# Performance work log

Hardware: AMD Instinct MI355X
Metric: run time of the kernel (lower is better)

## Reference

```python
import jax, jax.numpy as jnp
import numpy as np

E = 1024
H = 16
D = E // H  # head_dim = 64


def setup_inputs() -> dict:
    key = jax.random.key(0)
    ks = jax.random.split(key, 9)
    s = 1.0 / np.sqrt(E)
    inp = {
        "x": jax.random.normal(ks[0], (4, 2048, E), dtype=jnp.float32),
        "Wq": jax.random.uniform(ks[1], (E, E), jnp.float32, -s, s),
        "bq": jax.random.uniform(ks[2], (E,), jnp.float32, -s, s),
        "Wk": jax.random.uniform(ks[3], (E, E), jnp.float32, -s, s),
        "bk": jax.random.uniform(ks[4], (E,), jnp.float32, -s, s),
        "Wv": jax.random.uniform(ks[5], (E, E), jnp.float32, -s, s),
        "bv": jax.random.uniform(ks[6], (E,), jnp.float32, -s, s),
        "Wo": jax.random.uniform(ks[7], (E, E), jnp.float32, -s, s),
        "bo": jax.random.uniform(ks[8], (E,), jnp.float32, -s, s),
    }
    return inp


def reference(x, Wq, bq, Wk, bk, Wv, bv, Wo, bo):
    B, S, _ = x.shape
    scale = D ** -0.5
    # projections (torch Linear: x @ W.T + b), reshape to [B,H,S,D]
    def proj(W, b):
        y = jnp.einsum('bse,fe->bsf', x, W) + b
        return y.reshape(B, S, H, D).transpose(0, 2, 1, 3)
    q = proj(Wq, bq)
    k = proj(Wk, bk)
    v = proj(Wv, bv)
    scores = jnp.einsum('bhsd,bhtd->bhst', q, k) * scale  # [B,H,S,S]
    attn = jax.nn.softmax(scores, axis=-1)
    ctx = jnp.einsum('bhst,bhtd->bhsd', attn, v)  # [B,H,S,D]
    ctx = ctx.transpose(0, 2, 1, 3).reshape(B, S, E)
    out = jnp.einsum('bse,fe->bsf', ctx, Wo) + bo
    attn_avg = attn.mean(axis=1)  # [B,S,S]
    return out, attn_avg
```

## Files before the change

### kernel.cpp

```cpp
#include <hip/hip_runtime.h>
#include <math.h>

#define B_ 4
#define S_ 2048
#define E_ 1024
#define H_ 16
#define D_ 64

typedef __attribute__((ext_vector_type(8))) short bf16x8;
typedef __attribute__((ext_vector_type(4))) short bf16x4;
typedef __attribute__((ext_vector_type(4))) float f32x4;

#define MFMA(a, b, c) __builtin_amdgcn_mfma_f32_16x16x32_bf16((a), (b), (c), 0, 0, 0)

static __device__ __forceinline__ short f2bf(float f) {
    unsigned u = __float_as_uint(f);
    unsigned r = (u + 0x7FFFu + ((u >> 16) & 1u)) >> 16;
    return (short)r;
}

template <int MODE>
__launch_bounds__(256)
__global__ void gemm_mfma(const float* __restrict__ Af,
                          const short* __restrict__ Ab,
                          const float* __restrict__ W0, const float* __restrict__ b0,
                          short* __restrict__ o0,
                          const float* __restrict__ W1, const float* __restrict__ b1,
                          short* __restrict__ o1,
                          const float* __restrict__ W2, const float* __restrict__ b2,
                          short* __restrict__ o2,
                          float* __restrict__ of)
{
    const float* W = W0; const float* bias = b0; short* ob = o0;
    const int z = blockIdx.z;
    if (MODE == 0) {
        if (z == 1) { W = W1; bias = b1; ob = o1; }
        else if (z == 2) { W = W2; bias = b2; ob = o2; }
    }

    __shared__ short a_lds[128][72];
    __shared__ short b_lds[128][72];

    const int tid = threadIdx.x;
    const int l = tid & 63, w = tid >> 6;
    const int wm = w >> 1, wn = w & 1;
    const int lr = l & 15, lg = l >> 4;
    const int m0 = blockIdx.y * 128, f0 = blockIdx.x * 128;

    f32x4 acc[4][4];
#pragma unroll
    for (int i = 0; i < 4; ++i)
#pragma unroll
        for (int j = 0; j < 4; ++j) { acc[i][j][0] = 0.f; acc[i][j][1] = 0.f; acc[i][j][2] = 0.f; acc[i][j][3] = 0.f; }

    for (int k0 = 0; k0 < E_; k0 += 64) {
        __syncthreads();
        if (MODE == 0) {
#pragma unroll
            for (int i = 0; i < 8; ++i) {
                int idx = tid + i * 256;
                int row = idx >> 4, c4 = (idx & 15) * 4;
                float4 t = *(const float4*)&Af[(size_t)(m0 + row) * E_ + k0 + c4];
                bf16x4 v; v[0] = f2bf(t.x); v[1] = f2bf(t.y); v[2] = f2bf(t.z); v[3] = f2bf(t.w);
                *(bf16x4*)&a_lds[row][c4] = v;
            }
        } else {
#pragma unroll
            for (int i = 0; i < 4; ++i) {
                int idx = tid + i * 256;
                int row = idx >> 3, c8 = (idx & 7) * 8;
                *(bf16x8*)&a_lds[row][c8] = *(const bf16x8*)&Ab[(size_t)(m0 + row) * E_ + k0 + c8];
            }
        }
#pragma unroll
        for (int i = 0; i < 8; ++i) {
            int idx = tid + i * 256;
            int row = idx >> 4, c4 = (idx & 15) * 4;
            float4 t = *(const float4*)&W[(size_t)(f0 + row) * E_ + k0 + c4];
            bf16x4 v; v[0] = f2bf(t.x); v[1] = f2bf(t.y); v[2] = f2bf(t.z); v[3] = f2bf(t.w);
            *(bf16x4*)&b_lds[row][c4] = v;
        }
        __syncthreads();

        bf16x8 a[4][2];
#pragma unroll
        for (int mt = 0; mt < 4; ++mt)
#pragma unroll
            for (int c = 0; c < 2; ++c)
                a[mt][c] = *(const bf16x8*)&a_lds[wm * 64 + mt * 16 + lr][c * 32 + lg * 8];
#pragma unroll
        for (int nt = 0; nt < 4; ++nt) {
            bf16x8 bq0 = *(const bf16x8*)&b_lds[wn * 64 + nt * 16 + lr][lg * 8];
            bf16x8 bq1 = *(const bf16x8*)&b_lds[wn * 64 + nt * 16 + lr][32 + lg * 8];
#pragma unroll
            for (int mt = 0; mt < 4; ++mt) {
                acc[mt][nt] = MFMA(a[mt][0], bq0, acc[mt][nt]);
                acc[mt][nt] = MFMA(a[mt][1], bq1, acc[mt][nt]);
            }
        }
    }

    float bv[4];
#pragma unroll
    for (int nt = 0; nt < 4; ++nt) bv[nt] = bias[f0 + wn * 64 + nt * 16 + lr];

#pragma unroll
    for (int mt = 0; mt < 4; ++mt)
#pragma unroll
        for (int nt = 0; nt < 4; ++nt)
#pragma unroll
            for (int r = 0; r < 4; ++r) {
                const int m = m0 + wm * 64 + mt * 16 + lg * 4 + r;
                const int f = f0 + wn * 64 + nt * 16 + lr;
                float val = acc[mt][nt][r] + bv[nt];
                if (MODE == 0) {
                    const int bb = m >> 11, ss = m & (S_ - 1);
                    const int h = f >> 6, d = f & 63;
                    if (z == 0)
                        ob[((size_t)(bb * H_ + h) * S_ + ss) * D_ + d] = f2bf(val * 0.125f);
                    else if (z == 1)
                        ob[((size_t)(bb * H_ + h) * S_ + ss) * D_ + d] = f2bf(val);
                    else
                        ob[((size_t)(bb * H_ + h) * D_ + d) * S_ + ss] = f2bf(val);
                } else {
                    of[(size_t)m * E_ + f] = val;
                }
            }
}

__launch_bounds__(256)
__global__ void flash_mfma(const short* __restrict__ q, const short* __restrict__ k,
                           const short* __restrict__ vt, short* __restrict__ ctx,
                           float* __restrict__ mbuf, float* __restrict__ lbuf)
{
    __shared__ short k_lds[64][72];
    __shared__ short vt_lds[64][72];
    __shared__ short p_lds[64][72];

    const int tid = threadIdx.x;
    const int l = tid & 63, w = tid >> 6;
    const int lr = l & 15, lg = l >> 4;
    const int s0 = blockIdx.x * 64;
    const int bh = blockIdx.y;

    const short* qb  = q  + (size_t)bh * S_ * D_;
    const short* kb  = k  + (size_t)bh * S_ * D_;
    const short* vtb = vt + (size_t)bh * D_ * S_;

    bf16x8 qa[2];
#pragma unroll
    for (int c = 0; c < 2; ++c)
        qa[c] = *(const bf16x8*)&qb[(size_t)(s0 + w * 16 + lr) * D_ + c * 32 + lg * 8];

    float m_run[4], l_run[4];
    f32x4 cacc[4];
#pragma unroll
    for (int r = 0; r < 4; ++r) { m_run[r] = -1e30f; l_run[r] = 0.f; }
#pragma unroll
    for (int dt = 0; dt < 4; ++dt) { cacc[dt][0] = 0.f; cacc[dt][1] = 0.f; cacc[dt][2] = 0.f; cacc[dt][3] = 0.f; }

    for (int t0 = 0; t0 < S_; t0 += 64) {
        __syncthreads();
#pragma unroll
        for (int i = 0; i < 2; ++i) {
            int idx = tid + i * 256;
            int row = idx >> 3, c8 = (idx & 7) * 8;
            *(bf16x8*)&k_lds[row][c8]  = *(const bf16x8*)&kb[(size_t)(t0 + row) * D_ + c8];
            *(bf16x8*)&vt_lds[row][c8] = *(const bf16x8*)&vtb[(size_t)row * S_ + t0 + c8];
        }
        __syncthreads();

        f32x4 sc[4];
#pragma unroll
        for (int nt = 0; nt < 4; ++nt) {
            sc[nt][0] = 0.f; sc[nt][1] = 0.f; sc[nt][2] = 0.f; sc[nt][3] = 0.f;
            bf16x8 k0f = *(const bf16x8*)&k_lds[nt * 16 + lr][lg * 8];
            bf16x8 k1f = *(const bf16x8*)&k_lds[nt * 16 + lr][32 + lg * 8];
            sc[nt] = MFMA(qa[0], k0f, sc[nt]);
            sc[nt] = MFMA(qa[1], k1f, sc[nt]);
        }

#pragma unroll
        for (int r = 0; r < 4; ++r) {
            float mt_ = fmaxf(fmaxf(sc[0][r], sc[1][r]), fmaxf(sc[2][r], sc[3][r]));
#pragma unroll
            for (int off = 1; off < 16; off <<= 1)
                mt_ = fmaxf(mt_, __shfl_xor(mt_, off, 16));
            const float mn = fmaxf(m_run[r], mt_);
            const float al = __expf(m_run[r] - mn);
            float sig = 0.f;
#pragma unroll
            for (int nt = 0; nt < 4; ++nt) {
                float p = __expf(sc[nt][r] - mn);
                sig += p;
                p_lds[w * 16 + lg * 4 + r][nt * 16 + lr] = f2bf(p);
            }
#pragma unroll
            for (int off = 1; off < 16; off <<= 1)
                sig += __shfl_xor(sig, off, 16);
            m_run[r] = mn;
            l_run[r] = l_run[r] * al + sig;
#pragma unroll
            for (int dt = 0; dt < 4; ++dt) cacc[dt][r] *= al;
        }

        bf16x8 pa[2];
#pragma unroll
        for (int c = 0; c < 2; ++c)
            pa[c] = *(const bf16x8*)&p_lds[w * 16 + lr][c * 32 + lg * 8];
#pragma unroll
        for (int dt = 0; dt < 4; ++dt) {
            bf16x8 v0f = *(const bf16x8*)&vt_lds[dt * 16 + lr][lg * 8];
            bf16x8 v1f = *(const bf16x8*)&vt_lds[dt * 16 + lr][32 + lg * 8];
            cacc[dt] = MFMA(pa[0], v0f, cacc[dt]);
            cacc[dt] = MFMA(pa[1], v1f, cacc[dt]);
        }
    }

    const int b = bh >> 4, h = bh & 15;
#pragma unroll
    for (int r = 0; r < 4; ++r) {
        const float linv = 1.f / l_run[r];
        const int srow = s0 + w * 16 + lg * 4 + r;
#pragma unroll
        for (int dt = 0; dt < 4; ++dt)
            ctx[((size_t)(b * S_ + srow)) * E_ + h * D_ + dt * 16 + lr] = f2bf(cacc[dt][r] * linv);
        if (lr == 0) {
            mbuf[(size_t)bh * S_ + srow] = m_run[r];
            lbuf[(size_t)bh * S_ + srow] = l_run[r];
        }
    }
}

__launch_bounds__(256)
__global__ void avg_mfma(const short* __restrict__ q, const short* __restrict__ k,
                         const float* __restrict__ mbuf, const float* __restrict__ lbuf,
                         float* __restrict__ avg)
{
    __shared__ short qs[128][72];
    __shared__ short ks[128][72];

    const int tid = threadIdx.x;
    const int l = tid & 63, w = tid >> 6;
    const int lr = l & 15, lg = l >> 4;
    const int b = blockIdx.z;
    const int s0 = blockIdx.y * 128;
    const int t0 = blockIdx.x * 128;

    f32x4 acc[2][8];
#pragma unroll
    for (int mt = 0; mt < 2; ++mt)
#pragma unroll
        for (int nt = 0; nt < 8; ++nt) { acc[mt][nt][0] = 0.f; acc[mt][nt][1] = 0.f; acc[mt][nt][2] = 0.f; acc[mt][nt][3] = 0.f; }

    for (int h = 0; h < H_; ++h) {
        const int bh = b * H_ + h;
        const short* qb = q + (size_t)bh * S_ * D_;
        const short* kb = k + (size_t)bh * S_ * D_;
        __syncthreads();
#pragma unroll
        for (int i = 0; i < 4; ++i) {
            int idx = tid + i * 256;
            int row = idx >> 3, c8 = (idx & 7) * 8;
            *(bf16x8*)&qs[row][c8] = *(const bf16x8*)&qb[(size_t)(s0 + row) * D_ + c8];
            *(bf16x8*)&ks[row][c8] = *(const bf16x8*)&kb[(size_t)(t0 + row) * D_ + c8];
        }
        __syncthreads();

#pragma unroll
        for (int mt = 0; mt < 2; ++mt) {
            bf16x8 qa0 = *(const bf16x8*)&qs[w * 32 + mt * 16 + lr][lg * 8];
            bf16x8 qa1 = *(const bf16x8*)&qs[w * 32 + mt * 16 + lr][32 + lg * 8];
            float mv[4], li[4];
#pragma unroll
            for (int r = 0; r < 4; ++r) {
                const int srow = s0 + w * 32 + mt * 16 + lg * 4 + r;
                mv[r] = mbuf[(size_t)bh * S_ + srow];
                li[r] = 1.f / lbuf[(size_t)bh * S_ + srow];
            }
#pragma unroll
            for (int nt = 0; nt < 8; ++nt) {
                bf16x8 kb0 = *(const bf16x8*)&ks[nt * 16 + lr][lg * 8];
                bf16x8 kb1 = *(const bf16x8*)&ks[nt * 16 + lr][32 + lg * 8];
                f32x4 sv; sv[0] = 0.f; sv[1] = 0.f; sv[2] = 0.f; sv[3] = 0.f;
                sv = MFMA(qa0, kb0, sv);
                sv = MFMA(qa1, kb1, sv);
#pragma unroll
                for (int r = 0; r < 4; ++r)
                    acc[mt][nt][r] += __expf(sv[r] - mv[r]) * li[r];
            }
        }
    }

#pragma unroll
    for (int mt = 0; mt < 2; ++mt)
#pragma unroll
        for (int nt = 0; nt < 8; ++nt)
#pragma unroll
            for (int r = 0; r < 4; ++r) {
                const int srow = s0 + w * 32 + mt * 16 + lg * 4 + r;
                avg[((size_t)(b * S_ + srow)) * S_ + t0 + nt * 16 + lr] = acc[mt][nt][r] * 0.0625f;
            }
}

extern "C" void kernel_launch(void* const* d_in, const int* in_sizes, int n_in,
                              void* d_out, int out_size, void* d_ws, size_t ws_size,
                              hipStream_t stream)
{
    const float* x  = (const float*)d_in[0];
    const float* Wq = (const float*)d_in[1];
    const float* bq = (const float*)d_in[2];
    const float* Wk = (const float*)d_in[3];
    const float* bk = (const float*)d_in[4];
    const float* Wv = (const float*)d_in[5];
    const float* bv = (const float*)d_in[6];
    const float* Wo = (const float*)d_in[7];
    const float* bo = (const float*)d_in[8];

    float* out = (float*)d_out;
    float* avg = out + (size_t)B_ * S_ * E_;

    short* qw   = (short*)d_ws;
    short* kw   = qw + (size_t)B_ * H_ * S_ * D_;
    short* vtw  = kw + (size_t)B_ * H_ * S_ * D_;
    short* ctxw = vtw + (size_t)B_ * H_ * S_ * D_;
    float* mb   = (float*)(ctxw + (size_t)B_ * S_ * E_);
    float* lb   = mb + (size_t)B_ * H_ * S_;

    gemm_mfma<0><<<dim3(E_ / 128, (B_ * S_) / 128, 3), 256, 0, stream>>>(
        x, nullptr, Wq, bq, qw, Wk, bk, kw, Wv, bv, vtw, nullptr);

    flash_mfma<<<dim3(S_ / 64, B_ * H_), 256, 0, stream>>>(qw, kw, vtw, ctxw, mb, lb);

    gemm_mfma<1><<<dim3(E_ / 128, (B_ * S_) / 128, 1), 256, 0, stream>>>(
        nullptr, ctxw, Wo, bo, nullptr,
        nullptr, nullptr, nullptr, nullptr, nullptr, nullptr, out);

    avg_mfma<<<dim3(S_ / 128, S_ / 128, B_), 256, 0, stream>>>(qw, kw, mb, lb, avg);
}
```

Measured before the change: 631.6 us.

## Pre-convert inputs to bf16, use exp2 softmax with lazy rescale and swizzled P

Adds a separate kernel that converts x and all four weight matrices to bf16 once, so the GEMMs load bf16 tiles directly instead of converting fp32 per tile for every block. Folds log2(e) into the Q scale so softmax uses native exp2. Adds a lazy rescale in flash attention that skips the alpha update unless the running max grows by more than 8. Also XOR-swizzles the P tile in LDS to cut bank conflicts and uses rcp for reciprocals. The cost is an extra conversion pass plus workspace, and ctx now reuses the xb buffer.

After: 602.4 us. 4.6% less time.

```diff
diff --git a/kernel.cpp b/kernel.cpp
--- a/kernel.cpp
+++ b/kernel.cpp
@@ -1,4 +1,5 @@
 #include <hip/hip_runtime.h>
+#include <hip/hip_bf16.h>
 #include <math.h>
 
 #define B_ 4
@@ -8,30 +9,67 @@
 #define D_ 64
 
 typedef __attribute__((ext_vector_type(8))) short bf16x8;
-typedef __attribute__((ext_vector_type(4))) short bf16x4;
 typedef __attribute__((ext_vector_type(4))) float f32x4;
 
 #define MFMA(a, b, c) __builtin_amdgcn_mfma_f32_16x16x32_bf16((a), (b), (c), 0, 0, 0)
 
+#if __has_builtin(__builtin_amdgcn_exp2f)
+#define EXP2(x) __builtin_amdgcn_exp2f(x)
+#else
+#define EXP2(x) __expf(0.69314718f * (x))
+#endif
+
+#if __has_builtin(__builtin_amdgcn_rcpf)
+#define RCP(x) __builtin_amdgcn_rcpf(x)
+#else
+#define RCP(x) (1.0f / (x))
+#endif
+
+#define QSCALE 0.18033688011112042f
+
 static __device__ __forceinline__ short f2bf(float f) {
-    unsigned u = __float_as_uint(f);
-    unsigned r = (u + 0x7FFFu + ((u >> 16) & 1u)) >> 16;
-    return (short)r;
+    __hip_bfloat16 h = __float2bfloat16(f);
+    return *reinterpret_cast<short*>(&h);
+}
+
+__launch_bounds__(256)
+__global__ void cvt_bf16_5(const float* __restrict__ x,  const float* __restrict__ wq,
+                           const float* __restrict__ wk, const float* __restrict__ wv,
+                           const float* __restrict__ wo,
+                           short* __restrict__ xb,  short* __restrict__ wqb,
+                           short* __restrict__ wkb, short* __restrict__ wvb,
+                           short* __restrict__ wob)
+{
+    const int z = blockIdx.y;
+    const float* src; short* dst; int n;
+    if (z == 0)      { src = x;  dst = xb;  n = B_ * S_ * E_; }
+    else if (z == 1) { src = wq; dst = wqb; n = E_ * E_; }
+    else if (z == 2) { src = wk; dst = wkb; n = E_ * E_; }
+    else if (z == 3) { src = wv; dst = wvb; n = E_ * E_; }
+    else             { src = wo; dst = wob; n = E_ * E_; }
+
+    for (int base = (blockIdx.x * 256 + threadIdx.x) * 8; base < n; base += 512 * 256 * 8) {
+        float4 a = *(const float4*)&src[base];
+        float4 b = *(const float4*)&src[base + 4];
+        bf16x8 v;
+        v[0] = f2bf(a.x); v[1] = f2bf(a.y); v[2] = f2bf(a.z); v[3] = f2bf(a.w);
+        v[4] = f2bf(b.x); v[5] = f2bf(b.y); v[6] = f2bf(b.z); v[7] = f2bf(b.w);
+        *(bf16x8*)&dst[base] = v;
+    }
 }
 
 template <int MODE>
 __launch_bounds__(256)
-__global__ void gemm_mfma(const float* __restrict__ Af,
-                          const short* __restrict__ Ab,
-                          const float* __restrict__ W0, const float* __restrict__ b0,
+__global__ void gemm_mfma(const short* __restrict__ A,
+                          const short* __restrict__ W0, const float* __restrict__ b0,
                           short* __restrict__ o0,
-                          const float* __restrict__ W1, const float* __restrict__ b1,
+                          const short* __restrict__ W1, const float* __restrict__ b1,
                           short* __restrict__ o1,
-                          const float* __restrict__ W2, const float* __restrict__ b2,
+                          const short* __restrict__ W2, const float* __restrict__ b2,
                           short* __restrict__ o2,
                           float* __restrict__ of)
 {
-    const float* W = W0; const float* bias = b0; short* ob = o0;
+    const short* W = W0; const float* bias = b0; short* ob = o0;
     const int z = blockIdx.z;
     if (MODE == 0) {
         if (z == 1) { W = W1; bias = b1; ob = o1; }
@@ -55,30 +93,12 @@
 
     for (int k0 = 0; k0 < E_; k0 += 64) {
         __syncthreads();
-        if (MODE == 0) {
-#pragma unroll
-            for (int i = 0; i < 8; ++i) {
-                int idx = tid + i * 256;
-                int row = idx >> 4, c4 = (idx & 15) * 4;
-                float4 t = *(const float4*)&Af[(size_t)(m0 + row) * E_ + k0 + c4];
-                bf16x4 v; v[0] = f2bf(t.x); v[1] = f2bf(t.y); v[2] = f2bf(t.z); v[3] = f2bf(t.w);
-                *(bf16x4*)&a_lds[row][c4] = v;
-            }
-        } else {
-#pragma unroll
-            for (int i = 0; i < 4; ++i) {
-                int idx = tid + i * 256;
-                int row = idx >> 3, c8 = (idx & 7) * 8;
-                *(bf16x8*)&a_lds[row][c8] = *(const bf16x8*)&Ab[(size_t)(m0 + row) * E_ + k0 + c8];
-            }
-        }
-#pragma unroll
-        for (int i = 0; i < 8; ++i) {
+#pragma unroll
+        for (int i = 0; i < 4; ++i) {
             int idx = tid + i * 256;
-            int row = idx >> 4, c4 = (idx & 15) * 4;
-            float4 t = *(const float4*)&W[(size_t)(f0 + row) * E_ + k0 + c4];
-            bf16x4 v; v[0] = f2bf(t.x); v[1] = f2bf(t.y); v[2] = f2bf(t.z); v[3] = f2bf(t.w);
-            *(bf16x4*)&b_lds[row][c4] = v;
+            int row = idx >> 3, c8 = (idx & 7) * 8;
+            *(bf16x8*)&a_lds[row][c8] = *(const bf16x8*)&A[(size_t)(m0 + row) * E_ + k0 + c8];
+            *(bf16x8*)&b_lds[row][c8] = *(const bf16x8*)&W[(size_t)(f0 + row) * E_ + k0 + c8];
         }
         __syncthreads();
 
@@ -117,7 +137,7 @@
                     const int bb = m >> 11, ss = m & (S_ - 1);
                     const int h = f >> 6, d = f & 63;
                     if (z == 0)
-                        ob[((size_t)(bb * H_ + h) * S_ + ss) * D_ + d] = f2bf(val * 0.125f);
+                        ob[((size_t)(bb * H_ + h) * S_ + ss) * D_ + d] = f2bf(val * QSCALE);
                     else if (z == 1)
                         ob[((size_t)(bb * H_ + h) * S_ + ss) * D_ + d] = f2bf(val);
                     else
@@ -180,34 +200,51 @@
             sc[nt] = MFMA(qa[1], k1f, sc[nt]);
         }
 
+        float mt4[4];
 #pragma unroll
         for (int r = 0; r < 4; ++r) {
-            float mt_ = fmaxf(fmaxf(sc[0][r], sc[1][r]), fmaxf(sc[2][r], sc[3][r]));
+            float m_ = fmaxf(fmaxf(sc[0][r], sc[1][r]), fmaxf(sc[2][r], sc[3][r]));
 #pragma unroll
             for (int off = 1; off < 16; off <<= 1)
-                mt_ = fmaxf(mt_, __shfl_xor(mt_, off, 16));
-            const float mn = fmaxf(m_run[r], mt_);
-            const float al = __expf(m_run[r] - mn);
+                m_ = fmaxf(m_, __shfl_xor(m_, off, 16));
+            mt4[r] = m_;
+        }
+
+        const float need = fmaxf(fmaxf(mt4[0] - m_run[0], mt4[1] - m_run[1]),
+                                 fmaxf(mt4[2] - m_run[2], mt4[3] - m_run[3]));
+        if (!__all(need <= 8.0f)) {
+#pragma unroll
+            for (int r = 0; r < 4; ++r) {
+                const float mn = fmaxf(m_run[r], mt4[r]);
+                const float al = EXP2(m_run[r] - mn);
+                m_run[r] = mn;
+                l_run[r] *= al;
+#pragma unroll
+                for (int dt = 0; dt < 4; ++dt) cacc[dt][r] *= al;
+            }
+        }
+
+#pragma unroll
+        for (int r = 0; r < 4; ++r) {
+            const int prow = w * 16 + lg * 4 + r;
             float sig = 0.f;
 #pragma unroll
             for (int nt = 0; nt < 4; ++nt) {
-                float p = __expf(sc[nt][r] - mn);
+                float p = EXP2(sc[nt][r] - m_run[r]);
                 sig += p;
-                p_lds[w * 16 + lg * 4 + r][nt * 16 + lr] = f2bf(p);
+                p_lds[prow][(nt * 16 + lr) ^ (lg << 4)] = f2bf(p);
             }
 #pragma unroll
             for (int off = 1; off < 16; off <<= 1)
                 sig += __shfl_xor(sig, off, 16);
-            m_run[r] = mn;
-            l_run[r] = l_run[r] * al + sig;
-#pragma unroll
-            for (int dt = 0; dt < 4; ++dt) cacc[dt][r] *= al;
-        }
-
+            l_run[r] += sig;
+        }
+
+        const int xr = (lr >> 2) << 4;
         bf16x8 pa[2];
 #pragma unroll
         for (int c = 0; c < 2; ++c)
-            pa[c] = *(const bf16x8*)&p_lds[w * 16 + lr][c * 32 + lg * 8];
+            pa[c] = *(const bf16x8*)&p_lds[w * 16 + lr][(c * 32 + lg * 8) ^ xr];
 #pragma unroll
         for (int dt = 0; dt < 4; ++dt) {
             bf16x8 v0f = *(const bf16x8*)&vt_lds[dt * 16 + lr][lg * 8];
@@ -220,7 +257,7 @@
     const int b = bh >> 4, h = bh & 15;
 #pragma unroll
     for (int r = 0; r < 4; ++r) {
-        const float linv = 1.f / l_run[r];
+        const float linv = RCP(l_run[r]);
         const int srow = s0 + w * 16 + lg * 4 + r;
 #pragma unroll
         for (int dt = 0; dt < 4; ++dt)
@@ -276,7 +313,7 @@
             for (int r = 0; r < 4; ++r) {
                 const int srow = s0 + w * 32 + mt * 16 + lg * 4 + r;
                 mv[r] = mbuf[(size_t)bh * S_ + srow];
-                li[r] = 1.f / lbuf[(size_t)bh * S_ + srow];
+                li[r] = RCP(lbuf[(size_t)bh * S_ + srow]);
             }
 #pragma unroll
             for (int nt = 0; nt < 8; ++nt) {
@@ -287,7 +324,7 @@
                 sv = MFMA(qa1, kb1, sv);
 #pragma unroll
                 for (int r = 0; r < 4; ++r)
-                    acc[mt][nt][r] += __expf(sv[r] - mv[r]) * li[r];
+                    acc[mt][nt][r] += EXP2(sv[r] - mv[r]) * li[r];
             }
         }
     }
@@ -320,21 +357,33 @@
     float* out = (float*)d_out;
     float* avg = out + (size_t)B_ * S_ * E_;
 
-    short* qw   = (short*)d_ws;
-    short* kw   = qw + (size_t)B_ * H_ * S_ * D_;
-    short* vtw  = kw + (size_t)B_ * H_ * S_ * D_;
-    short* ctxw = vtw + (size_t)B_ * H_ * S_ * D_;
-    float* mb   = (float*)(ctxw + (size_t)B_ * S_ * E_);
+    const size_t NX = (size_t)B_ * S_ * E_;
+    const size_t NW = (size_t)E_ * E_;
+    const size_t NQ = (size_t)B_ * H_ * S_ * D_;
+
+    short* xb   = (short*)d_ws;
+    short* wqb  = xb  + NX;
+    short* wkb  = wqb + NW;
+    short* wvb  = wkb + NW;
+    short* wob  = wvb + NW;
+    short* qw   = wob + NW;
+    short* kw   = qw  + NQ;
+    short* vtw  = kw  + NQ;
+    float* mb   = (float*)(vtw + NQ);
     float* lb   = mb + (size_t)B_ * H_ * S_;
+    short* ctxw = xb;
+
+    cvt_bf16_5<<<dim3(512, 5), 256, 0, stream>>>(x, Wq, Wk, Wv, Wo,
+                                                 xb, wqb, wkb, wvb, wob);
 
     gemm_mfma<0><<<dim3(E_ / 128, (B_ * S_) / 128, 3), 256, 0, stream>>>(
-        x, nullptr, Wq, bq, qw, Wk, bk, kw, Wv, bv, vtw, nullptr);
+        xb, wqb, bq, qw, wkb, bk, kw, wvb, bv, vtw, nullptr);
 
     flash_mfma<<<dim3(S_ / 64, B_ * H_), 256, 0, stream>>>(qw, kw, vtw, ctxw, mb, lb);
 
     gemm_mfma<1><<<dim3(E_ / 128, (B_ * S_) / 128, 1), 256, 0, stream>>>(
-        nullptr, ctxw, Wo, bo, nullptr,
-        nullptr, nullptr, nullptr, nullptr, nullptr, nullptr, out);
+        ctxw, wob, bo, nullptr, nullptr, nullptr, nullptr,
+        nullptr, nullptr, nullptr, out);
 
     avg_mfma<<<dim3(S_ / 128, S_ / 128, B_), 256, 0, stream>>>(qw, kw, mb, lb, avg);
 }
```
